# Performance work log

Measured on AMD Instinct MI355X. Metric: run time of the kernel, lower is better.

The kernel has to match this reference:

```python
import jax, jax.numpy as jnp
import numpy as np

D = 1024
H = 16
DK = D // H
FF = int(8 / 3 * D)  # 2730
EPS = 1e-6


def setup_inputs() -> dict:
    key = jax.random.key(0)
    ks = jax.random.split(key, 8)
    s = lambda n: 1.0 / np.sqrt(n)
    return {
        "x": jax.random.normal(ks[0], (2, 2048, D), dtype=jnp.float32),
        "w_qkv": jax.random.normal(ks[1], (3 * D, D), dtype=jnp.float32) * s(D),
        "w_o": jax.random.normal(ks[2], (D, D), dtype=jnp.float32) * s(D),
        "n1_w": jnp.ones((D,), dtype=jnp.float32),
        "n2_w": jnp.ones((D,), dtype=jnp.float32),
        "w1": jax.random.normal(ks[3], (FF, D), dtype=jnp.float32) * s(D),
        "w2": jax.random.normal(ks[4], (D, FF), dtype=jnp.float32) * s(FF),
        "w3": jax.random.normal(ks[5], (FF, D), dtype=jnp.float32) * s(D),
    }


def _rmsnorm(x, w):
    return x * jax.lax.rsqrt(jnp.mean(x * x, axis=-1, keepdims=True) + EPS) * w


def _attn(x, w_qkv, w_o):
    B, L, _ = x.shape
    qkv = x @ w_qkv.T                       # [B,L,3D]
    qkv = qkv.reshape(B, L, 3, H, DK)
    q, k, v = qkv[:, :, 0], qkv[:, :, 1], qkv[:, :, 2]   # [B,L,H,DK]
    scores = jnp.einsum("blhd,bmhd->bhlm", q, k) / np.sqrt(DK).astype(np.float32)
    attn = jax.nn.softmax(scores, axis=-1)               # [B,H,L,L]
    out = jnp.einsum("bhlm,bmhd->blhd", attn, v).reshape(B, L, D)
    return out @ w_o.T


def _swiglu(x, w1, w2, w3):
    return (jax.nn.silu(x @ w1.T) * (x @ w3.T)) @ w2.T


def reference(x, w_qkv, w_o, n1_w, n2_w, w1, w2, w3):
    x = x + _attn(_rmsnorm(x, n1_w), w_qkv, w_o)
    return x + _swiglu(_rmsnorm(x, n2_w), w1, w2, w3)
```

## Files before the change

kernel.cpp:

```cpp
#include <hip/hip_runtime.h>
#include <stdint.h>


#define LSEQ   2048
#define DMODEL 1024
#define NHEAD  16
#define NTOK   4096
#define FFR    2730
#define FFP    2816
#define FF2    5632

typedef short  short8  __attribute__((ext_vector_type(8)));
typedef float  floatx4 __attribute__((ext_vector_type(4)));

__device__ __forceinline__ uint16_t f2bf(float f) {
  uint32_t u = __builtin_bit_cast(uint32_t, f);
  u += 0x7FFFu + ((u >> 16) & 1u);
  return (uint16_t)(u >> 16);
}
__device__ __forceinline__ uint32_t cvt_pk_bf16(float a, float b) {
  uint32_t d;
  asm("v_cvt_pk_bf16_f32 %0, %1, %2" : "=v"(d) : "v"(a), "v"(b));
  return d;
}
__device__ __forceinline__ void gl2lds16(const void* g, void* l) {
  __builtin_amdgcn_global_load_lds(
      (const __attribute__((address_space(1))) unsigned int*)g,
      (__attribute__((address_space(3))) unsigned int*)l, 16, 0, 0);
}

__global__ __launch_bounds__(256) void cvt_all_k(const float* __restrict__ wqkv,
                                                 const float* __restrict__ wo,
                                                 const float* __restrict__ w1,
                                                 const float* __restrict__ w3,
                                                 uint16_t* __restrict__ dst) {
  int g = blockIdx.x;
  int c = threadIdx.x * 4;
  const float* src = nullptr;
  if (g < 3072)       src = wqkv + (size_t)g * 1024;
  else if (g < 4096)  src = wo + (size_t)(g - 3072) * 1024;
  else {
    int r = g - 4096;
    int u = r >> 6, wi = r & 63;
    int srow = u * 32 + (wi & 31);
    if (srow < FFR) src = ((wi < 32) ? w1 : w3) + (size_t)srow * 1024;
  }
  float4 v = src ? *(const float4*)(src + c) : float4{0, 0, 0, 0};
  uint64_t pack =  (uint64_t)f2bf(v.x)        | ((uint64_t)f2bf(v.y) << 16)
                | ((uint64_t)f2bf(v.z) << 32) | ((uint64_t)f2bf(v.w) << 48);
  *(uint64_t*)(dst + (size_t)g * 1024 + c) = pack;
}

__global__ __launch_bounds__(256) void cvt_pad_k(const float* __restrict__ src,
                                                 uint16_t* __restrict__ dst,
                                                 int rows, int cols, int cols_p) {
  long idx = (long)blockIdx.x * 256 + threadIdx.x;
  int c4 = cols_p >> 2;
  if (idx >= (long)rows * c4) return;
  int r = (int)(idx / c4);
  int c = (int)(idx % c4) * 4;
  uint64_t pack;
  if (c + 3 < cols) {
    const float* sp = src + (size_t)r * cols + c;
    float2 a = *(const float2*)sp;
    float2 b2 = *(const float2*)(sp + 2);
    pack =  (uint64_t)f2bf(a.x)        | ((uint64_t)f2bf(a.y) << 16)
         | ((uint64_t)f2bf(b2.x) << 32) | ((uint64_t)f2bf(b2.y) << 48);
  } else {
    pack = 0;
    for (int e = 0; e < 4; e++) {
      float v = (c + e < cols) ? src[(size_t)r * cols + c + e] : 0.0f;
      pack |= (uint64_t)f2bf(v) << (16 * e);
    }
  }
  *(uint64_t*)(dst + (size_t)r * cols_p + c) = pack;
}

__global__ __launch_bounds__(256) void rmsnorm_k(const float* __restrict__ x,
                                                 const float* __restrict__ wgt,
                                                 uint16_t* __restrict__ out) {
  const int row = blockIdx.x;
  const int c = threadIdx.x * 4;
  const float* xr = x + (size_t)row * DMODEL;
  float4 v = *(const float4*)(xr + c);
  float ss = v.x * v.x + v.y * v.y + v.z * v.z + v.w * v.w;
#pragma unroll
  for (int off = 32; off >= 1; off >>= 1) ss += __shfl_down(ss, off, 64);
  __shared__ float red[4];
  if ((threadIdx.x & 63) == 0) red[threadIdx.x >> 6] = ss;
  __syncthreads();
  float tot = red[0] + red[1] + red[2] + red[3];
  float scale = rsqrtf(tot * (1.0f / DMODEL) + 1e-6f);
  float4 wv = *(const float4*)(wgt + c);
  uint64_t pack =  (uint64_t)f2bf(v.x * scale * wv.x)
                | ((uint64_t)f2bf(v.y * scale * wv.y) << 16)
                | ((uint64_t)f2bf(v.z * scale * wv.z) << 32)
                | ((uint64_t)f2bf(v.w * scale * wv.w) << 48);
  *(uint64_t*)(out + (size_t)row * DMODEL + c) = pack;
}

template <int MODE, int TM, int TN>
__global__ __launch_bounds__(256) void gemm_bt(const uint16_t* __restrict__ A,
                                               const uint16_t* __restrict__ B,
                                               uint16_t* __restrict__ Cb,
                                               float* __restrict__ Cf,
                                               const float* __restrict__ Res,
                                               int M, int N, int K) {
  constexpr int FI = TM / 32, FJ = TN / 32;
  constexpr int NIT = (TM + TN) / 64;
  __shared__ uint16_t As[TM * 32];
  __shared__ uint16_t Bs[TN * 32];
  const int tid = threadIdx.x;
  const int w = tid >> 6, lane = tid & 63;
  const int grp = lane >> 4, l16 = lane & 15;
  const int m0 = blockIdx.y * TM, n0 = blockIdx.x * TN;
  const int rw = (w >> 1) * (TM / 2), cw = (w & 1) * (TN / 2);

  floatx4 acc[FI][FJ] = {};

  const uint16_t* gp[NIT];
  uint16_t* lp[NIT];
#pragma unroll
  for (int i = 0; i < NIT; i++) {
    int c = i * 256 + tid;
    if (c < TM * 4) {
      gp[i] = A + (size_t)(m0 + (c >> 2)) * K + (c & 3) * 8;
      lp[i] = As + c * 8;
    } else {
      int c2 = c - TM * 4;
      gp[i] = B + (size_t)(n0 + (c2 >> 2)) * K + (c2 & 3) * 8;
      lp[i] = Bs + c2 * 8;
    }
  }

  for (int k0 = 0; k0 < K; k0 += 32) {
#pragma unroll
    for (int i = 0; i < NIT; i++) gl2lds16(gp[i] + k0, lp[i]);
    __syncthreads();
    short8 af[FI], bfr[FJ];
#pragma unroll
    for (int i = 0; i < FI; i++)
      af[i] = *(const short8*)(As + (rw + i * 16 + l16) * 32 + grp * 8);
#pragma unroll
    for (int j = 0; j < FJ; j++)
      bfr[j] = *(const short8*)(Bs + (cw + j * 16 + l16) * 32 + grp * 8);
#pragma unroll
    for (int i = 0; i < FI; i++)
#pragma unroll
      for (int j = 0; j < FJ; j++)
        acc[i][j] = __builtin_amdgcn_mfma_f32_16x16x32_bf16(af[i], bfr[j], acc[i][j], 0, 0, 0);
    __syncthreads();
  }

  if constexpr (MODE == 2) {
    const int half = N >> 1;
#pragma unroll
    for (int i = 0; i < FI; i++) {
      const int mrow = m0 + rw + i * 16 + grp * 4;
#pragma unroll
      for (int j = 0; j < 2; j++) {
        const int gcol = (n0 >> 1) + (cw >> 1) + j * 16 + l16;
#pragma unroll
        for (int r = 0; r < 4; r++) {
          float a = acc[i][j][r];
          float bv = acc[i][j + 2][r];
          float ex = __builtin_amdgcn_exp2f(-a * 1.4426950408889634f);
          float s = a * __builtin_amdgcn_rcpf(1.0f + ex);
          Cb[(size_t)(mrow + r) * half + gcol] = f2bf(s * bv);
        }
      }
    }
  } else {
#pragma unroll
    for (int i = 0; i < FI; i++) {
#pragma unroll
      for (int j = 0; j < FJ; j++) {
        const int mrow = m0 + rw + i * 16 + grp * 4;
        const int ncol = n0 + cw + j * 16 + l16;
#pragma unroll
        for (int r = 0; r < 4; r++) {
          size_t idx = (size_t)(mrow + r) * N + ncol;
          float v = acc[i][j][r];
          if (MODE == 0) Cb[idx] = f2bf(v);
          else           Cf[idx] = v + Res[idx];
        }
      }
    }
  }
}

__global__ __launch_bounds__(256, 2) void attn_flash(const uint16_t* __restrict__ qkv,
                                                     uint16_t* __restrict__ outp) {
  const int tid = threadIdx.x;
  const int w = tid >> 6, lane = tid & 63;
  const int grp = lane >> 4, l16 = lane & 15;
  const int lin = blockIdx.x;
  const int xcd = lin & 7;
  const int slot = lin >> 3;
  const int pair = xcd * 4 + (slot >> 4);
  const int qc = slot & 15;
  const int h = pair & 15, b = pair >> 4;
  const int q0 = qc * 128;

  __shared__ uint16_t Ks[2][4096];
  __shared__ uint16_t Vt[2][64 * 72];
  __shared__ uint16_t Ps[128 * 72];

  const size_t base = ((size_t)b * LSEQ) * 3072 + (size_t)h * 64;

  short8 aq[2][2];
#pragma unroll
  for (int fi = 0; fi < 2; fi++) {
    const uint16_t* qr = qkv + base + (size_t)(q0 + w * 32 + fi * 16 + l16) * 3072;
    aq[fi][0] = *(const short8*)(qr + grp * 8);
    aq[fi][1] = *(const short8*)(qr + 32 + grp * 8);
  }

#pragma unroll
  for (int i = 0; i < 2; i++) {
    int c = i * 256 + tid;
    int row = c >> 3, cc = (c & 7) ^ (row & 7);
    gl2lds16(qkv + base + (size_t)row * 3072 + 1024 + cc * 8, Ks[0] + c * 8);
  }
#pragma unroll
  for (int i = 0; i < 2; i++) {
    int c = i * 256 + tid;
    int tt = c & 63, db = c >> 6;
    uint4 vv = *(const uint4*)(qkv + base + (size_t)tt * 3072 + 2048 + db * 8);
    uint32_t uu[4] = {vv.x, vv.y, vv.z, vv.w};
#pragma unroll
    for (int e = 0; e < 4; e++) {
      Vt[0][(db * 8 + e * 2 + 0) * 72 + tt] = (uint16_t)(uu[e] & 0xFFFFu);
      Vt[0][(db * 8 + e * 2 + 1) * 72 + tt] = (uint16_t)(uu[e] >> 16);
    }
  }
  __syncthreads();

  float lsum[2] = {};
  floatx4 o_acc[2][4] = {};
  const float C = 0.125f * 1.4426950408889634f;

  for (int kc = 0; kc < LSEQ / 64; kc++) {
    const int cur = kc & 1, nxt = cur ^ 1;
    const bool pre = (kc + 1 < LSEQ / 64);
    const int t1 = (kc + 1) * 64;
    uint4 vv[2];
    if (pre) {
#pragma unroll
      for (int i = 0; i < 2; i++) {
        int c = i * 256 + tid;
        int row = c >> 3, cc = (c & 7) ^ (row & 7);
        gl2lds16(qkv + base + (size_t)(t1 + row) * 3072 + 1024 + cc * 8, Ks[nxt] + c * 8);
      }
#pragma unroll
      for (int i = 0; i < 2; i++) {
        int c = i * 256 + tid;
        int tt = c & 63, db = c >> 6;
        vv[i] = *(const uint4*)(qkv + base + (size_t)(t1 + tt) * 3072 + 2048 + db * 8);
      }
    }

    floatx4 s_acc[4][2] = {};
    __builtin_amdgcn_s_setprio(1);
#pragma unroll
    for (int j = 0; j < 4; j++) {
      const int krow = j * 16 + l16;
#pragma unroll
      for (int kk = 0; kk < 2; kk++) {
        int cc = kk * 4 + grp;
        short8 bk = *(const short8*)(Ks[cur] + (krow * 8 + (cc ^ (krow & 7))) * 8);
#pragma unroll
        for (int fi = 0; fi < 2; fi++)
          s_acc[j][fi] = __builtin_amdgcn_mfma_f32_16x16x32_bf16(bk, aq[fi][kk], s_acc[j][fi], 0, 0, 0);
      }
    }
    __builtin_amdgcn_s_setprio(0);

#pragma unroll
    for (int j = 0; j < 4; j++)
#pragma unroll
      for (int fi = 0; fi < 2; fi++) {
        float p0 = __builtin_amdgcn_exp2f(s_acc[j][fi][0] * C);
        float p1 = __builtin_amdgcn_exp2f(s_acc[j][fi][1] * C);
        float p2 = __builtin_amdgcn_exp2f(s_acc[j][fi][2] * C);
        float p3 = __builtin_amdgcn_exp2f(s_acc[j][fi][3] * C);
        lsum[fi] += (p0 + p1) + (p2 + p3);
        uint2 pk;
        pk.x = cvt_pk_bf16(p0, p1);
        pk.y = cvt_pk_bf16(p2, p3);
        *(uint2*)(Ps + (w * 32 + fi * 16 + l16) * 72 + j * 16 + grp * 4) = pk;
      }

    __builtin_amdgcn_s_setprio(1);
#pragma unroll
    for (int kk = 0; kk < 2; kk++) {
      short8 ap0 = *(const short8*)(Ps + (w * 32 + l16) * 72 + kk * 32 + grp * 8);
      short8 ap1 = *(const short8*)(Ps + (w * 32 + 16 + l16) * 72 + kk * 32 + grp * 8);
#pragma unroll
      for (int jj = 0; jj < 4; jj++) {
        short8 bv = *(const short8*)(Vt[cur] + (jj * 16 + l16) * 72 + kk * 32 + grp * 8);
        o_acc[0][jj] = __builtin_amdgcn_mfma_f32_16x16x32_bf16(ap0, bv, o_acc[0][jj], 0, 0, 0);
        o_acc[1][jj] = __builtin_amdgcn_mfma_f32_16x16x32_bf16(ap1, bv, o_acc[1][jj], 0, 0, 0);
      }
    }
    __builtin_amdgcn_s_setprio(0);

    if (pre) {
#pragma unroll
      for (int i = 0; i < 2; i++) {
        int c = i * 256 + tid;
        int tt = c & 63, db = c >> 6;
        uint32_t uu[4] = {vv[i].x, vv[i].y, vv[i].z, vv[i].w};
#pragma unroll
        for (int e = 0; e < 4; e++) {
          Vt[nxt][(db * 8 + e * 2 + 0) * 72 + tt] = (uint16_t)(uu[e] & 0xFFFFu);
          Vt[nxt][(db * 8 + e * 2 + 1) * 72 + tt] = (uint16_t)(uu[e] >> 16);
        }
      }
    }
    __syncthreads();
  }

#pragma unroll
  for (int fi = 0; fi < 2; fi++) {
    lsum[fi] += __shfl_xor(lsum[fi], 16, 64);
    lsum[fi] += __shfl_xor(lsum[fi], 32, 64);
  }
  float lsr[2][4];
#pragma unroll
  for (int fi = 0; fi < 2; fi++)
#pragma unroll
    for (int r = 0; r < 4; r++)
      lsr[fi][r] = __shfl(lsum[fi], grp * 4 + r, 64);
#pragma unroll
  for (int fi = 0; fi < 2; fi++)
#pragma unroll
    for (int jj = 0; jj < 4; jj++)
#pragma unroll
      for (int r = 0; r < 4; r++) {
        int row = b * LSEQ + q0 + w * 32 + fi * 16 + grp * 4 + r;
        float o = o_acc[fi][jj][r] * __builtin_amdgcn_rcpf(lsr[fi][r]);
        outp[(size_t)row * DMODEL + h * 64 + jj * 16 + l16] = f2bf(o);
      }
}

extern "C" void kernel_launch(void* const* d_in, const int* in_sizes, int n_in,
                              void* d_out, int out_size, void* d_ws, size_t ws_size,
                              hipStream_t stream) {
  const float* x    = (const float*)d_in[0];
  const float* wqkv = (const float*)d_in[1];
  const float* wo   = (const float*)d_in[2];
  const float* n1w  = (const float*)d_in[3];
  const float* n2w  = (const float*)d_in[4];
  const float* w1   = (const float*)d_in[5];
  const float* w2   = (const float*)d_in[6];
  const float* w3   = (const float*)d_in[7];
  float* out = (float*)d_out;

  char* p = (char*)d_ws;
  uint16_t* wall  = (uint16_t*)p; p += (size_t)9728 * 1024 * 2;
  uint16_t* wqkvb = wall;
  uint16_t* wob   = wall + (size_t)3072 * 1024;
  uint16_t* w13b  = wall + (size_t)4096 * 1024;
  uint16_t* w2b   = (uint16_t*)p; p += (size_t)1024 * FFP * 2;
  uint16_t* h1    = (uint16_t*)p; p += (size_t)NTOK * DMODEL * 2;
  uint16_t* qkvb  = (uint16_t*)p; p += (size_t)NTOK * 3072 * 2;
  uint16_t* attno = (uint16_t*)p; p += (size_t)NTOK * DMODEL * 2;
  float*    x1    = (float*)p;    p += (size_t)NTOK * DMODEL * 4;
  uint16_t* h2    = (uint16_t*)p; p += (size_t)NTOK * DMODEL * 2;
  uint16_t* gbuf  = (uint16_t*)p; p += (size_t)NTOK * FFP * 2;

  cvt_all_k<<<9728, 256, 0, stream>>>(wqkv, wo, w1, w3, wall);
  cvt_pad_k<<<(1024 * (FFP / 4)) / 256, 256, 0, stream>>>(w2, w2b, 1024, FFR, FFP);

  rmsnorm_k<<<NTOK, 256, 0, stream>>>(x, n1w, h1);
  gemm_bt<0, 128, 128><<<dim3(3072 / 128, NTOK / 128), 256, 0, stream>>>(
      h1, wqkvb, qkvb, nullptr, nullptr, NTOK, 3072, 1024);
  attn_flash<<<512, 256, 0, stream>>>(qkvb, attno);
  gemm_bt<1, 128, 64><<<dim3(1024 / 64, NTOK / 128), 256, 0, stream>>>(
      attno, wob, nullptr, x1, x, NTOK, 1024, 1024);
  rmsnorm_k<<<NTOK, 256, 0, stream>>>(x1, n2w, h2);
  gemm_bt<2, 128, 128><<<dim3(FF2 / 128, NTOK / 128), 256, 0, stream>>>(
      h2, w13b, gbuf, nullptr, nullptr, NTOK, FF2, 1024);
  gemm_bt<1, 128, 64><<<dim3(1024 / 64, NTOK / 128), 256, 0, stream>>>(
      gbuf, w2b, nullptr, out, x1, NTOK, 1024, FFP);
}
```

Measured before the change: 368.6 us.

## Double-buffer GEMM LDS tiles with async global-to-LDS prefetch

Replaces the single-buffered GEMM main loop with a two-stage ping-pong LDS buffer. The next K-tile's global_load_lds is issued before the current tile is computed, with explicit vmcnt waits and barriers, so memory latency overlaps the MFMA work. LDS use doubles, which may lower occupancy, and vm_wait only handles NIT values of 3 or 4, so other tile configurations would wait incorrectly.

Result: faster. 341.1 us (-7.5%).

```diff
diff --git a/kernel.cpp b/kernel.cpp
--- a/kernel.cpp
+++ b/kernel.cpp
@@ -27,6 +27,12 @@
   __builtin_amdgcn_global_load_lds(
       (const __attribute__((address_space(1))) unsigned int*)g,
       (__attribute__((address_space(3))) unsigned int*)l, 16, 0, 0);
+}
+template <int N>
+__device__ __forceinline__ void vm_wait() {
+  if constexpr (N == 0)      asm volatile("s_waitcnt vmcnt(0)" ::: "memory");
+  else if constexpr (N == 3) asm volatile("s_waitcnt vmcnt(3)" ::: "memory");
+  else if constexpr (N == 4) asm volatile("s_waitcnt vmcnt(4)" ::: "memory");
 }
 
 __global__ __launch_bounds__(256) void cvt_all_k(const float* __restrict__ wqkv,
@@ -108,8 +114,8 @@
                                                int M, int N, int K) {
   constexpr int FI = TM / 32, FJ = TN / 32;
   constexpr int NIT = (TM + TN) / 64;
-  __shared__ uint16_t As[TM * 32];
-  __shared__ uint16_t Bs[TN * 32];
+  constexpr int BUFO = (TM + TN) * 32;
+  __shared__ uint16_t S[2 * BUFO];
   const int tid = threadIdx.x;
   const int w = tid >> 6, lane = tid & 63;
   const int grp = lane >> 4, l16 = lane & 15;
@@ -125,31 +131,64 @@
     int c = i * 256 + tid;
     if (c < TM * 4) {
       gp[i] = A + (size_t)(m0 + (c >> 2)) * K + (c & 3) * 8;
-      lp[i] = As + c * 8;
+      lp[i] = S + c * 8;
     } else {
       int c2 = c - TM * 4;
       gp[i] = B + (size_t)(n0 + (c2 >> 2)) * K + (c2 & 3) * 8;
-      lp[i] = Bs + c2 * 8;
-    }
-  }
-
-  for (int k0 = 0; k0 < K; k0 += 32) {
-#pragma unroll
-    for (int i = 0; i < NIT; i++) gl2lds16(gp[i] + k0, lp[i]);
-    __syncthreads();
+      lp[i] = S + TM * 32 + c2 * 8;
+    }
+  }
+
+  const int nt = K / 32;
+
+  auto stage = [&](int t, int buf) {
+#pragma unroll
+    for (int i = 0; i < NIT; i++) gl2lds16(gp[i] + t * 32, lp[i] + buf * BUFO);
+  };
+  auto compute = [&](int buf) {
+    const uint16_t* Sb = S + buf * BUFO;
     short8 af[FI], bfr[FJ];
 #pragma unroll
     for (int i = 0; i < FI; i++)
-      af[i] = *(const short8*)(As + (rw + i * 16 + l16) * 32 + grp * 8);
+      af[i] = *(const short8*)(Sb + (rw + i * 16 + l16) * 32 + grp * 8);
 #pragma unroll
     for (int j = 0; j < FJ; j++)
-      bfr[j] = *(const short8*)(Bs + (cw + j * 16 + l16) * 32 + grp * 8);
+      bfr[j] = *(const short8*)(Sb + TM * 32 + (cw + j * 16 + l16) * 32 + grp * 8);
 #pragma unroll
     for (int i = 0; i < FI; i++)
 #pragma unroll
       for (int j = 0; j < FJ; j++)
         acc[i][j] = __builtin_amdgcn_mfma_f32_16x16x32_bf16(af[i], bfr[j], acc[i][j], 0, 0, 0);
-    __syncthreads();
+  };
+
+  stage(0, 0);
+  stage(1, 1);
+  __builtin_amdgcn_sched_barrier(0);
+  vm_wait<NIT>();
+  __builtin_amdgcn_sched_barrier(0);
+  __builtin_amdgcn_s_barrier();
+  __builtin_amdgcn_sched_barrier(0);
+
+  for (int t = 0;;) {
+    compute(0);
+    if (++t == nt) break;
+    __builtin_amdgcn_s_barrier();
+    __builtin_amdgcn_sched_barrier(0);
+    if (t + 1 < nt) { stage(t + 1, 0); __builtin_amdgcn_sched_barrier(0); vm_wait<NIT>(); }
+    else            vm_wait<0>();
+    __builtin_amdgcn_sched_barrier(0);
+    __builtin_amdgcn_s_barrier();
+    __builtin_amdgcn_sched_barrier(0);
+
+    compute(1);
+    if (++t == nt) break;
+    __builtin_amdgcn_s_barrier();
+    __builtin_amdgcn_sched_barrier(0);
+    if (t + 1 < nt) { stage(t + 1, 1); __builtin_amdgcn_sched_barrier(0); vm_wait<NIT>(); }
+    else            vm_wait<0>();
+    __builtin_amdgcn_sched_barrier(0);
+    __builtin_amdgcn_s_barrier();
+    __builtin_amdgcn_sched_barrier(0);
   }
 
   if constexpr (MODE == 2) {
```
